# Performance work log

Measured on AMD Instinct MI355X. Metric: run time of the kernel, lower is better.

The kernel has to match this reference:

```python
import jax, jax.numpy as jnp
import numpy as np

B, NORB, N_UP, N_DN, HIDDEN = 1024, 128, 32, 32, 4096


def setup_inputs() -> dict:
    rng = np.random.default_rng(0)
    # Build valid occupancy configs: exactly N_UP up-electrons (bit 0) and
    # N_DN down-electrons (bit 1) per sample. Encoding: 0=empty,1=up,2=dn,3=updn.
    up_order = np.argsort(rng.random((B, NORB)), axis=1)
    dn_order = np.argsort(rng.random((B, NORB)), axis=1)
    up_bit = np.zeros((B, NORB), np.int32)
    dn_bit = np.zeros((B, NORB), np.int32)
    np.put_along_axis(up_bit, up_order[:, :N_UP], 1, axis=1)
    np.put_along_axis(dn_bit, dn_order[:, :N_DN], 1, axis=1)
    x = jnp.asarray(up_bit + 2 * dn_bit, dtype=jnp.int32)

    key = jax.random.key(0)
    k1, k2, k3 = jax.random.split(key, 3)
    orbitals = jax.random.normal(k1, (NORB, N_UP), jnp.float32)
    W1 = jax.random.normal(k2, (4 * NORB, HIDDEN), jnp.float32) / np.sqrt(4 * NORB)
    b1 = jnp.zeros((HIDDEN,), jnp.float32)
    W2 = jax.random.normal(k3, (HIDDEN, NORB * N_UP), jnp.float32) / np.sqrt(HIDDEN)
    b2 = jnp.zeros((NORB * N_UP,), jnp.float32)
    return {"x": x, "orbitals": orbitals, "W1": W1, "b1": b1, "W2": W2, "b2": b2}


def _occupancies_to_electrons(x, n_up, n_dn):
    # Per-spin sorted positions of occupied orbitals. Stable argsort on the
    # inverted mask keeps occupied sites first, in ascending orbital order.
    up_mask = (x & 1) == 1
    dn_mask = (x & 2) == 2
    y_up = jnp.argsort(jnp.where(up_mask, 0, 1), axis=-1, stable=True)[:, :n_up]
    y_dn = jnp.argsort(jnp.where(dn_mask, 0, 1), axis=-1, stable=True)[:, :n_dn]
    return y_up, y_dn


def reference(x, orbitals, W1, b1, W2, b2):
    Bsz, norb = x.shape
    n_up = orbitals.shape[1]

    # correction_fun: MLP on one-hot config -> [B, norb, n_up]
    h = jax.nn.one_hot(x, 4, dtype=W1.dtype).reshape(Bsz, -1)  # [B, 4*norb]
    h = jax.nn.relu(h @ W1 + b1)                               # [B, hidden]
    corrections = (h @ W2 + b2).reshape(Bsz, norb, n_up)       # [B, norb, n_up]

    y_up, y_dn = _occupancies_to_electrons(x, n_up, n_up)
    y_up = y_up[..., None]  # [B, n_up, 1]
    y_dn = y_dn[..., None]

    # gather orbital rows + correction rows per electron (spin-symmetric orbitals)
    phi_up = jnp.take_along_axis(orbitals[None], y_up, axis=1)  # [B, n_up, n_up]
    phi_dn = jnp.take_along_axis(orbitals[None], y_dn, axis=1)
    d_up = jnp.take_along_axis(corrections, y_up, axis=1)
    d_dn = jnp.take_along_axis(corrections, y_dn, axis=1)

    s_up, log_det_up = jnp.linalg.slogdet(phi_up + d_up)
    s_dn, log_det_dn = jnp.linalg.slogdet(phi_dn + d_dn)
    return log_det_up + log_det_dn + jnp.log(s_up * s_dn + 0j)  # complex [B]
```

## Files before the change

kernel.cpp:

```cpp
#include <hip/hip_runtime.h>
#include <cmath>

#define B_SZ  1024
#define NORB  128
#define NUP   32
#define HID   4096
#define NCORR (NORB * NUP)
#define K1    (4 * NORB)

typedef short    bf16x8 __attribute__((ext_vector_type(8)));
typedef _Float16 f16x8  __attribute__((ext_vector_type(8)));
typedef float    f32x4  __attribute__((ext_vector_type(4)));

__device__ __forceinline__ unsigned short f2bf_rne(float f) {
    unsigned int u = __float_as_uint(f);
    u += 0x7FFFu + ((u >> 16) & 1u);
    return (unsigned short)(u >> 16);
}

__global__ __launch_bounds__(256) void k_splitW(const float* __restrict__ W,
                                                unsigned short* __restrict__ Bph,
                                                unsigned short* __restrict__ Bpl,
                                                int ktTot) {
    __shared__ float tile[64][33];
    int n0 = blockIdx.x * 32, k0 = blockIdx.y * 64;
    int t = threadIdx.x;

    int rl = t >> 3, c4 = (t & 7) * 4;
#pragma unroll
    for (int i = 0; i < 2; ++i) {
        int kl = rl + 32 * i;
        float4 v = *(const float4*)(W + (size_t)(k0 + kl) * 4096 + n0 + c4);
        tile[kl][c4 + 0] = v.x; tile[kl][c4 + 1] = v.y;
        tile[kl][c4 + 2] = v.z; tile[kl][c4 + 3] = v.w;
    }
    __syncthreads();

    int nl = t & 31, kg = t >> 5;
    int nt = (n0 + nl) >> 4;
    int kt = (k0 >> 5) + (kg >> 2);
    int lane_o = (kg & 3) * 16 + (nl & 15);
    size_t o = (((size_t)nt * ktTot + kt) * 64 + lane_o) * 8;

    unsigned short hi8[8], lo8[8];
#pragma unroll
    for (int j = 0; j < 8; ++j) {
        float v = tile[kg * 8 + j][nl];
        unsigned short hi = f2bf_rne(v);
        float fhi = __uint_as_float((unsigned int)hi << 16);
        hi8[j] = hi;
        lo8[j] = f2bf_rne(v - fhi);
    }
    *(bf16x8*)(Bph + o) = *(bf16x8*)hi8;
    *(bf16x8*)(Bpl + o) = *(bf16x8*)lo8;
}

__global__ __launch_bounds__(256) void k_splitW16(const float* __restrict__ W,
                                                  _Float16* __restrict__ Bph,
                                                  _Float16* __restrict__ Bpl) {
    __shared__ float tile[64][33];
    int n0 = blockIdx.x * 32, k0 = blockIdx.y * 64;
    int t = threadIdx.x;

    int rl = t >> 3, c4 = (t & 7) * 4;
#pragma unroll
    for (int i = 0; i < 2; ++i) {
        int kl = rl + 32 * i;
        float4 v = *(const float4*)(W + (size_t)(k0 + kl) * 4096 + n0 + c4);
        tile[kl][c4 + 0] = v.x; tile[kl][c4 + 1] = v.y;
        tile[kl][c4 + 2] = v.z; tile[kl][c4 + 3] = v.w;
    }
    __syncthreads();

    int nl = t & 31, kg = t >> 5;
    int nt = (n0 + nl) >> 4;
    int kt = (k0 >> 5) + (kg >> 2);
    int lane_o = (kg & 3) * 16 + (nl & 15);
    size_t o = (((size_t)nt * 128 + kt) * 64 + lane_o) * 8;

    f16x8 hi8, lo8;
#pragma unroll
    for (int j = 0; j < 8; ++j) {
        float v = tile[kg * 8 + j][nl];
        _Float16 hi = (_Float16)v;
        hi8[j] = hi;
        lo8[j] = (_Float16)((v - (float)hi) * 2048.0f);
    }
    *(f16x8*)(Bph + o) = hi8;
    *(f16x8*)(Bpl + o) = lo8;
}

__global__ __launch_bounds__(256, 2) void k_hidden3(const int* __restrict__ x,
                                                    const unsigned short* __restrict__ Bph,
                                                    const unsigned short* __restrict__ Bpl,
                                                    const float* __restrict__ b1,
                                                    _Float16* __restrict__ h16) {
    __shared__ unsigned int sxp[64][8];
    __shared__ unsigned short BF[2][4][4][512];
    __shared__ float Ht[64][132];

    int n0 = blockIdx.x * 128;
    int m0 = blockIdx.y * 64;
    int t = threadIdx.x;
    int w = t >> 6, lane = t & 63;
    int lm = lane & 15, kq = lane >> 4;
    int wn = w * 32;

#pragma unroll
    for (int i = 0; i < 2; ++i) {
        int id = t + 256 * i;
        int row = id >> 3, d = id & 7;
        const int* src = x + (size_t)(m0 + row) * NORB + d * 16;
        unsigned int dw = 0;
#pragma unroll
        for (int b = 0; b < 16; ++b) dw |= ((unsigned int)(src[b] & 3)) << (2 * b);
        sxp[row][d] = dw;
    }

    int nt0 = (n0 + wn) >> 4;
    const unsigned short* bh0 = Bph + (size_t)nt0 * (16 * 512) + (size_t)lane * 8;
    const unsigned short* bh1 = Bph + (size_t)(nt0 + 1) * (16 * 512) + (size_t)lane * 8;
    const unsigned short* bl0 = Bpl + (size_t)nt0 * (16 * 512) + (size_t)lane * 8;
    const unsigned short* bl1 = Bpl + (size_t)(nt0 + 1) * (16 * 512) + (size_t)lane * 8;

    f32x4 acc[4][2] = {};

    bf16x8 r0 = *(const bf16x8*)(bh0);
    bf16x8 r1 = *(const bf16x8*)(bh1);
    bf16x8 r2 = *(const bf16x8*)(bl0);
    bf16x8 r3 = *(const bf16x8*)(bl1);
    bf16x8 r4 = *(const bf16x8*)(bh0 + 512);
    bf16x8 r5 = *(const bf16x8*)(bh1 + 512);
    bf16x8 r6 = *(const bf16x8*)(bl0 + 512);
    bf16x8 r7 = *(const bf16x8*)(bl1 + 512);

    __syncthreads();

    for (int p = 0; p < 8; ++p) {
        if (p) __syncthreads();

        *(bf16x8*)&BF[0][w][0][lane * 8] = r0;
        *(bf16x8*)&BF[0][w][1][lane * 8] = r1;
        *(bf16x8*)&BF[0][w][2][lane * 8] = r2;
        *(bf16x8*)&BF[0][w][3][lane * 8] = r3;
        *(bf16x8*)&BF[1][w][0][lane * 8] = r4;
        *(bf16x8*)&BF[1][w][1][lane * 8] = r5;
        *(bf16x8*)&BF[1][w][2][lane * 8] = r6;
        *(bf16x8*)&BF[1][w][3][lane * 8] = r7;
        __syncthreads();

        int kn = (p + 1 < 8) ? p + 1 : 7;
        r0 = *(const bf16x8*)(bh0 + (2 * kn) * 512);
        r1 = *(const bf16x8*)(bh1 + (2 * kn) * 512);
        r2 = *(const bf16x8*)(bl0 + (2 * kn) * 512);
        r3 = *(const bf16x8*)(bl1 + (2 * kn) * 512);
        r4 = *(const bf16x8*)(bh0 + (2 * kn + 1) * 512);
        r5 = *(const bf16x8*)(bh1 + (2 * kn + 1) * 512);
        r6 = *(const bf16x8*)(bl0 + (2 * kn + 1) * 512);
        r7 = *(const bf16x8*)(bl1 + (2 * kn + 1) * 512);

#pragma unroll
        for (int s = 0; s < 2; ++s) {
            int kt = 2 * p + s;
            int i0 = kt * 8 + kq * 2;
            int dwIdx = i0 >> 4;
            int sh = (i0 & 15) * 2;
            bf16x8 af[4];
#pragma unroll
            for (int fm = 0; fm < 4; ++fm) {
                unsigned int dw = sxp[fm * 16 + lm][dwIdx];
                unsigned int c01 = (dw >> sh) & 0xFu;
                union { bf16x8 v; unsigned long long u[2]; } a;
                a.u[0] = 0x3F80ULL << ((c01 & 3u) * 16);
                a.u[1] = 0x3F80ULL << ((c01 >> 2) * 16);
                af[fm] = a.v;
            }

            bf16x8 b0h = *(const bf16x8*)&BF[s][w][0][lane * 8];
            bf16x8 b1h = *(const bf16x8*)&BF[s][w][1][lane * 8];
            bf16x8 b0l = *(const bf16x8*)&BF[s][w][2][lane * 8];
            bf16x8 b1l = *(const bf16x8*)&BF[s][w][3][lane * 8];

#pragma unroll
            for (int fm = 0; fm < 4; ++fm) {
                acc[fm][0] = __builtin_amdgcn_mfma_f32_16x16x32_bf16(af[fm], b0h, acc[fm][0], 0, 0, 0);
                acc[fm][0] = __builtin_amdgcn_mfma_f32_16x16x32_bf16(af[fm], b0l, acc[fm][0], 0, 0, 0);
                acc[fm][1] = __builtin_amdgcn_mfma_f32_16x16x32_bf16(af[fm], b1h, acc[fm][1], 0, 0, 0);
                acc[fm][1] = __builtin_amdgcn_mfma_f32_16x16x32_bf16(af[fm], b1l, acc[fm][1], 0, 0, 0);
            }
        }
    }

    __syncthreads();
#pragma unroll
    for (int fm = 0; fm < 4; ++fm)
#pragma unroll
        for (int fn = 0; fn < 2; ++fn) {
            int n = wn + fn * 16 + lm;
            float bv = b1[n0 + n];
#pragma unroll
            for (int r = 0; r < 4; ++r)
                Ht[fm * 16 + kq * 4 + r][n] = fmaxf(acc[fm][fn][r] + bv, 0.f);
        }
    __syncthreads();

    size_t mt0 = (size_t)(m0 >> 4), kt0 = (size_t)(n0 >> 5);
#pragma unroll
    for (int fi = 0; fi < 4; ++fi) {
        int f = w * 4 + fi;
        int mt = f >> 2, ktn = f & 3;
        int m = mt * 16 + lm;
        int kn = ktn * 32 + kq * 8;
        float4 v0 = *(const float4*)&Ht[m][kn];
        float4 v1 = *(const float4*)&Ht[m][kn + 4];
        float vv[8] = {v0.x, v0.y, v0.z, v0.w, v1.x, v1.y, v1.z, v1.w};
        f16x8 o16;
#pragma unroll
        for (int j = 0; j < 8; ++j) o16[j] = (_Float16)vv[j];
        size_t o = (((mt0 + mt) * 128 + (kt0 + ktn)) * 64 + lane) * 8;
        *(f16x8*)(h16 + o) = o16;
    }
}

__global__ __launch_bounds__(256) void k_hidden_f32(const int* __restrict__ x,
                                                    const float* __restrict__ W1,
                                                    const float* __restrict__ b1,
                                                    float* __restrict__ h) {
    int b = blockIdx.x, tid = threadIdx.x;
    __shared__ int sx[NORB];
    if (tid < NORB) sx[tid] = x[b * NORB + tid];
    __syncthreads();
    float acc[16];
#pragma unroll
    for (int u = 0; u < 16; ++u) acc[u] = b1[tid + 256 * u];
    for (int i = 0; i < NORB; ++i) {
        const float* row = W1 + (size_t)(4 * i + sx[i]) * HID;
#pragma unroll
        for (int u = 0; u < 16; ++u) acc[u] += row[tid + 256 * u];
    }
    float* hb = h + (size_t)b * HID;
#pragma unroll
    for (int u = 0; u < 16; ++u) hb[tid + 256 * u] = fmaxf(acc[u], 0.f);
}

__global__ __launch_bounds__(256, 2) void k_gemm7(const _Float16* __restrict__ Ap,
                                                  const _Float16* __restrict__ Bph,
                                                  const _Float16* __restrict__ Bpl,
                                                  const float* __restrict__ bias,
                                                  float* __restrict__ C) {
    __shared__ _Float16 AF[2][4][512];

    int n0 = blockIdx.x * 128;
    int m0 = blockIdx.y * 64;
    int t = threadIdx.x;
    int w = t >> 6, lane = t & 63;
    int lm = lane & 15, kq = lane >> 4;
    int wn = w * 32;

    int mt0 = m0 >> 4;
    int nt0 = (n0 + wn) >> 4;

    const _Float16* ag  = Ap  + (size_t)(mt0 + w) * 65536 + (size_t)lane * 8;
    const _Float16* bh0 = Bph + (size_t)nt0 * 65536 + (size_t)lane * 8;
    const _Float16* bh1 = Bph + (size_t)(nt0 + 1) * 65536 + (size_t)lane * 8;
    const _Float16* bl0 = Bpl + (size_t)nt0 * 65536 + (size_t)lane * 8;
    const _Float16* bl1 = Bpl + (size_t)(nt0 + 1) * 65536 + (size_t)lane * 8;

    f32x4 accH[4][2] = {}, accL[4][2] = {};

    f16x8 r0 = *(const f16x8*)(ag);
    f16x8 r1 = *(const f16x8*)(ag + 512);

    for (int ktp = 0; ktp < 64; ++ktp) {
        if (ktp) __syncthreads();

        int o0 = (2 * ktp) * 512, o1 = o0 + 512;
        f16x8 B0h0 = *(const f16x8*)(bh0 + o0);
        f16x8 B0h1 = *(const f16x8*)(bh1 + o0);
        f16x8 B0l0 = *(const f16x8*)(bl0 + o0);
        f16x8 B0l1 = *(const f16x8*)(bl1 + o0);
        f16x8 B1h0 = *(const f16x8*)(bh0 + o1);
        f16x8 B1h1 = *(const f16x8*)(bh1 + o1);
        f16x8 B1l0 = *(const f16x8*)(bl0 + o1);
        f16x8 B1l1 = *(const f16x8*)(bl1 + o1);

        *(f16x8*)&AF[0][w][lane * 8] = r0;
        *(f16x8*)&AF[1][w][lane * 8] = r1;
        __syncthreads();

        int kn = (ktp + 1 < 64) ? ktp + 1 : 63;
        r0 = *(const f16x8*)(ag + (size_t)(2 * kn) * 512);
        r1 = *(const f16x8*)(ag + (size_t)(2 * kn + 1) * 512);

        f16x8 a0[4], a1[4];
#pragma unroll
        for (int fm = 0; fm < 4; ++fm) {
            a0[fm] = *(const f16x8*)&AF[0][fm][lane * 8];
            a1[fm] = *(const f16x8*)&AF[1][fm][lane * 8];
        }

#pragma unroll
        for (int fm = 0; fm < 4; ++fm) {
            accH[fm][0] = __builtin_amdgcn_mfma_f32_16x16x32_f16(a0[fm], B0h0, accH[fm][0], 0, 0, 0);
            accL[fm][0] = __builtin_amdgcn_mfma_f32_16x16x32_f16(a0[fm], B0l0, accL[fm][0], 0, 0, 0);
            accH[fm][1] = __builtin_amdgcn_mfma_f32_16x16x32_f16(a0[fm], B0h1, accH[fm][1], 0, 0, 0);
            accL[fm][1] = __builtin_amdgcn_mfma_f32_16x16x32_f16(a0[fm], B0l1, accL[fm][1], 0, 0, 0);
        }
#pragma unroll
        for (int fm = 0; fm < 4; ++fm) {
            accH[fm][0] = __builtin_amdgcn_mfma_f32_16x16x32_f16(a1[fm], B1h0, accH[fm][0], 0, 0, 0);
            accL[fm][0] = __builtin_amdgcn_mfma_f32_16x16x32_f16(a1[fm], B1l0, accL[fm][0], 0, 0, 0);
            accH[fm][1] = __builtin_amdgcn_mfma_f32_16x16x32_f16(a1[fm], B1h1, accH[fm][1], 0, 0, 0);
            accL[fm][1] = __builtin_amdgcn_mfma_f32_16x16x32_f16(a1[fm], B1l1, accL[fm][1], 0, 0, 0);
        }
    }

    const float ls = 1.0f / 2048.0f;
#pragma unroll
    for (int fm = 0; fm < 4; ++fm)
#pragma unroll
        for (int fn = 0; fn < 2; ++fn) {
            int n = n0 + wn + fn * 16 + lm;
            float bv = bias[n];
#pragma unroll
            for (int r = 0; r < 4; ++r) {
                int m = m0 + fm * 16 + kq * 4 + r;
                C[(size_t)m * NCORR + n] = accH[fm][fn][r] + ls * accL[fm][fn][r] + bv;
            }
        }
}

#define BM 64
#define BN 64
#define BK 32
__global__ __launch_bounds__(256) void k_gemm(const float* __restrict__ A,
                                              const float* __restrict__ Bm,
                                              const float* __restrict__ bias,
                                              float* __restrict__ C) {
    __shared__ float As[BK][68];
    __shared__ float Bs[BK][BN];
    int n0 = blockIdx.x * BN, m0 = blockIdx.y * BM;
    int tid = threadIdx.x;
    int tm = tid >> 4, tn = tid & 15;
    int am = tid >> 3, ak = (tid & 7) * 4;
    int bk = tid >> 4, bn = (tid & 15) * 4;
    float acc[4][4] = {};
    for (int k0 = 0; k0 < HID; k0 += BK) {
#pragma unroll
        for (int s = 0; s < 2; ++s) {
            int m = am + 32 * s;
            float4 v = *(const float4*)(A + (size_t)(m0 + m) * HID + k0 + ak);
            As[ak + 0][m] = v.x; As[ak + 1][m] = v.y;
            As[ak + 2][m] = v.z; As[ak + 3][m] = v.w;
        }
#pragma unroll
        for (int s = 0; s < 2; ++s) {
            int k = bk + 16 * s;
            float4 v = *(const float4*)(Bm + (size_t)(k0 + k) * NCORR + n0 + bn);
            *(float4*)&Bs[k][bn] = v;
        }
        __syncthreads();
#pragma unroll
        for (int kk = 0; kk < BK; ++kk) {
            float4 a = *(const float4*)&As[kk][tm * 4];
            float4 bv = *(const float4*)&Bs[kk][tn * 4];
            float av[4] = {a.x, a.y, a.z, a.w};
            float bb[4] = {bv.x, bv.y, bv.z, bv.w};
#pragma unroll
            for (int i = 0; i < 4; ++i)
#pragma unroll
                for (int j = 0; j < 4; ++j) acc[i][j] += av[i] * bb[j];
        }
        __syncthreads();
    }
#pragma unroll
    for (int i = 0; i < 4; ++i) {
        int m = m0 + tm * 4 + i;
        float4 o;
        o.x = acc[i][0] + bias[n0 + tn * 4 + 0];
        o.y = acc[i][1] + bias[n0 + tn * 4 + 1];
        o.z = acc[i][2] + bias[n0 + tn * 4 + 2];
        o.w = acc[i][3] + bias[n0 + tn * 4 + 3];
        *(float4*)(C + (size_t)m * NCORR + n0 + tn * 4) = o;
    }
}

__global__ __launch_bounds__(128) void k_det(const int* __restrict__ x,
                                             const float* __restrict__ orbitals,
                                             const float* __restrict__ corr,
                                             float* __restrict__ out,
                                             int imag_off) {
    int b = blockIdx.x, tid = threadIdx.x;
    __shared__ int sx[NORB];
    __shared__ int yup[NUP], ydn[NUP];
    __shared__ float M[2][NUP][NUP + 1];
    __shared__ float rlog[2];
    __shared__ int rneg[2];

    sx[tid] = x[b * NORB + tid];
    __syncthreads();

    int occ = sx[tid];
    if (occ & 1) {
        int r = 0;
        for (int i = 0; i < tid; ++i) r += sx[i] & 1;
        yup[r] = tid;
    }
    if (occ & 2) {
        int r = 0;
        for (int i = 0; i < tid; ++i) r += (sx[i] >> 1) & 1;
        ydn[r] = tid;
    }
    __syncthreads();

    const float* cb = corr + (size_t)b * NCORR;
    for (int idx = tid; idx < 2 * NUP * NUP; idx += 128) {
        int s = idx >> 10;
        int i = (idx >> 5) & 31;
        int j = idx & 31;
        int r = s ? ydn[i] : yup[i];
        M[s][i][j] = orbitals[r * NUP + j] + cb[r * NUP + j];
    }
    __syncthreads();

    int wv = tid >> 6, lane = tid & 63;
    float (*Mm)[NUP + 1] = M[wv];
    float logdet = 0.f;
    int neg = 0;

    for (int k = 0; k < NUP; ++k) {
        float v = (lane >= k && lane < NUP) ? fabsf(Mm[lane][k]) : -1.f;
        int pi = lane;
#pragma unroll
        for (int off = 32; off > 0; off >>= 1) {
            float v2 = __shfl_down(v, off);
            int p2 = __shfl_down(pi, off);
            if (v2 > v) { v = v2; pi = p2; }
        }
        int p = __shfl(pi, 0);

        if (p != k) {
            if (lane < NUP) {
                float t1 = Mm[k][lane];
                Mm[k][lane] = Mm[p][lane];
                Mm[p][lane] = t1;
            }
            neg ^= 1;
        }
        __syncthreads();

        float pv = Mm[k][k];
        logdet += logf(fabsf(pv));
        if (pv < 0.f) neg ^= 1;

        int row = k + 1 + (lane & 31);
        int half = lane >> 5;
        if (row < NUP) {
            float f = Mm[row][k] / pv;
            for (int j = k + 1 + half; j < NUP; j += 2)
                Mm[row][j] -= f * Mm[k][j];
        }
        __syncthreads();
    }

    if (lane == 0) { rlog[wv] = logdet; rneg[wv] = neg; }
    __syncthreads();
    if (tid == 0) {
        out[b] = rlog[0] + rlog[1];
        if (imag_off > 0)
            out[imag_off + b] =
                (rneg[0] ^ rneg[1]) ? 3.14159265358979323846f : 0.f;
    }
}

extern "C" void kernel_launch(void* const* d_in, const int* in_sizes, int n_in,
                              void* d_out, int out_size, void* d_ws, size_t ws_size,
                              hipStream_t stream) {
    const int*   x        = (const int*)d_in[0];
    const float* orbitals = (const float*)d_in[1];
    const float* W1       = (const float*)d_in[2];
    const float* b1       = (const float*)d_in[3];
    const float* W2       = (const float*)d_in[4];
    const float* b2       = (const float*)d_in[5];
    float* out = (float*)d_out;
    int imag_off = (out_size == 2 * B_SZ) ? B_SZ : 0;

    const size_t need = (size_t)96 * 1024 * 1024;
    if (ws_size >= need) {
        _Float16* h16  = (_Float16*)d_ws;
        _Float16* Bh16 = h16 + (size_t)B_SZ * HID;
        _Float16* Bl16 = Bh16 + (size_t)HID * NCORR;
        float*    corr = (float*)(Bl16 + (size_t)HID * NCORR);

        unsigned short* W1ph = (unsigned short*)corr;
        unsigned short* W1pl = W1ph + (size_t)K1 * HID;

        k_splitW<<<dim3(HID / 32, K1 / 64), 256, 0, stream>>>(W1, W1ph, W1pl, 16);
        k_splitW16<<<dim3(NCORR / 32, HID / 64), 256, 0, stream>>>(W2, Bh16, Bl16);

        k_hidden3<<<dim3(HID / 128, B_SZ / 64), 256, 0, stream>>>(x, W1ph, W1pl, b1, h16);

        dim3 g2(NCORR / 128, B_SZ / 64);
        k_gemm7<<<g2, 256, 0, stream>>>(h16, Bh16, Bl16, b2, corr);
        k_det<<<B_SZ, 128, 0, stream>>>(x, orbitals, corr, out, imag_off);
    } else {
        float* h    = (float*)d_ws;
        float* corr = h + (size_t)B_SZ * HID;
        k_hidden_f32<<<B_SZ, 256, 0, stream>>>(x, W1, b1, h);
        dim3 g2(NCORR / BN, B_SZ / BM);
        k_gemm<<<g2, 256, 0, stream>>>(h, W2, b2, corr);
        k_det<<<B_SZ, 128, 0, stream>>>(x, orbitals, corr, out, imag_off);
    }
}
```

Measured before the change: 242.5 us.

## Split GEMM block across 8 waves with double-buffered LDS A tiles

The second-layer GEMM now runs 512 threads per block, each wave owning one 16-column N tile instead of two. This halves per-wave accumulators and B-register loads to raise occupancy. The A tile in LDS is double-buffered so one __syncthreads per iteration is enough, and sched_barrier calls pin loads ahead of the MFMA chains, including in the hidden-layer kernel. The cost is more waves sharing each LDS A tile and a less flexible compiler schedule.

```diff
diff --git a/kernel.cpp b/kernel.cpp
--- a/kernel.cpp
+++ b/kernel.cpp
@@ -158,6 +158,7 @@
         r5 = *(const bf16x8*)(bh1 + (2 * kn + 1) * 512);
         r6 = *(const bf16x8*)(bl0 + (2 * kn + 1) * 512);
         r7 = *(const bf16x8*)(bl1 + (2 * kn + 1) * 512);
+        __builtin_amdgcn_sched_barrier(0);
 
 #pragma unroll
         for (int s = 0; s < 2; ++s) {
@@ -243,90 +244,75 @@
     for (int u = 0; u < 16; ++u) hb[tid + 256 * u] = fmaxf(acc[u], 0.f);
 }
 
-__global__ __launch_bounds__(256, 2) void k_gemm7(const _Float16* __restrict__ Ap,
+__global__ __launch_bounds__(512, 4) void k_gemm8(const _Float16* __restrict__ Ap,
                                                   const _Float16* __restrict__ Bph,
                                                   const _Float16* __restrict__ Bpl,
                                                   const float* __restrict__ bias,
                                                   float* __restrict__ C) {
-    __shared__ _Float16 AF[2][4][512];
+    __shared__ _Float16 AF[2][2][4][512];
 
     int n0 = blockIdx.x * 128;
     int m0 = blockIdx.y * 64;
     int t = threadIdx.x;
     int w = t >> 6, lane = t & 63;
     int lm = lane & 15, kq = lane >> 4;
-    int wn = w * 32;
 
     int mt0 = m0 >> 4;
-    int nt0 = (n0 + wn) >> 4;
-
-    const _Float16* ag  = Ap  + (size_t)(mt0 + w) * 65536 + (size_t)lane * 8;
-    const _Float16* bh0 = Bph + (size_t)nt0 * 65536 + (size_t)lane * 8;
-    const _Float16* bh1 = Bph + (size_t)(nt0 + 1) * 65536 + (size_t)lane * 8;
-    const _Float16* bl0 = Bpl + (size_t)nt0 * 65536 + (size_t)lane * 8;
-    const _Float16* bl1 = Bpl + (size_t)(nt0 + 1) * 65536 + (size_t)lane * 8;
-
-    f32x4 accH[4][2] = {}, accL[4][2] = {};
-
-    f16x8 r0 = *(const f16x8*)(ag);
-    f16x8 r1 = *(const f16x8*)(ag + 512);
+    int nt0 = (n0 >> 4) + w;
+
+    int sA = w & 1, mA = w >> 1;
+    const _Float16* ag = Ap  + (size_t)(mt0 + mA) * 65536 + (size_t)lane * 8;
+    const _Float16* bh = Bph + (size_t)nt0 * 65536 + (size_t)lane * 8;
+    const _Float16* bl = Bpl + (size_t)nt0 * 65536 + (size_t)lane * 8;
+
+    f32x4 accH[4] = {}, accL[4] = {};
+
+    f16x8 r = *(const f16x8*)(ag + (size_t)sA * 512);
 
     for (int ktp = 0; ktp < 64; ++ktp) {
-        if (ktp) __syncthreads();
-
-        int o0 = (2 * ktp) * 512, o1 = o0 + 512;
-        f16x8 B0h0 = *(const f16x8*)(bh0 + o0);
-        f16x8 B0h1 = *(const f16x8*)(bh1 + o0);
-        f16x8 B0l0 = *(const f16x8*)(bl0 + o0);
-        f16x8 B0l1 = *(const f16x8*)(bl1 + o0);
-        f16x8 B1h0 = *(const f16x8*)(bh0 + o1);
-        f16x8 B1h1 = *(const f16x8*)(bh1 + o1);
-        f16x8 B1l0 = *(const f16x8*)(bl0 + o1);
-        f16x8 B1l1 = *(const f16x8*)(bl1 + o1);
-
-        *(f16x8*)&AF[0][w][lane * 8] = r0;
-        *(f16x8*)&AF[1][w][lane * 8] = r1;
+        int buf = ktp & 1;
+        *(f16x8*)&AF[buf][sA][mA][lane * 8] = r;
         __syncthreads();
 
+        size_t oc = (size_t)(2 * ktp) * 512;
+        f16x8 B0h = *(const f16x8*)(bh + oc);
+        f16x8 B0l = *(const f16x8*)(bl + oc);
+        f16x8 B1h = *(const f16x8*)(bh + oc + 512);
+        f16x8 B1l = *(const f16x8*)(bl + oc + 512);
         int kn = (ktp + 1 < 64) ? ktp + 1 : 63;
-        r0 = *(const f16x8*)(ag + (size_t)(2 * kn) * 512);
-        r1 = *(const f16x8*)(ag + (size_t)(2 * kn + 1) * 512);
+        f16x8 nr = *(const f16x8*)(ag + (size_t)(2 * kn + sA) * 512);
+        __builtin_amdgcn_sched_barrier(0);
 
         f16x8 a0[4], a1[4];
 #pragma unroll
         for (int fm = 0; fm < 4; ++fm) {
-            a0[fm] = *(const f16x8*)&AF[0][fm][lane * 8];
-            a1[fm] = *(const f16x8*)&AF[1][fm][lane * 8];
+            a0[fm] = *(const f16x8*)&AF[buf][0][fm][lane * 8];
+            a1[fm] = *(const f16x8*)&AF[buf][1][fm][lane * 8];
         }
 
 #pragma unroll
         for (int fm = 0; fm < 4; ++fm) {
-            accH[fm][0] = __builtin_amdgcn_mfma_f32_16x16x32_f16(a0[fm], B0h0, accH[fm][0], 0, 0, 0);
-            accL[fm][0] = __builtin_amdgcn_mfma_f32_16x16x32_f16(a0[fm], B0l0, accL[fm][0], 0, 0, 0);
-            accH[fm][1] = __builtin_amdgcn_mfma_f32_16x16x32_f16(a0[fm], B0h1, accH[fm][1], 0, 0, 0);
-            accL[fm][1] = __builtin_amdgcn_mfma_f32_16x16x32_f16(a0[fm], B0l1, accL[fm][1], 0, 0, 0);
+            accH[fm] = __builtin_amdgcn_mfma_f32_16x16x32_f16(a0[fm], B0h, accH[fm], 0, 0, 0);
+            accL[fm] = __builtin_amdgcn_mfma_f32_16x16x32_f16(a0[fm], B0l, accL[fm], 0, 0, 0);
         }
 #pragma unroll
         for (int fm = 0; fm < 4; ++fm) {
-            accH[fm][0] = __builtin_amdgcn_mfma_f32_16x16x32_f16(a1[fm], B1h0, accH[fm][0], 0, 0, 0);
-            accL[fm][0] = __builtin_amdgcn_mfma_f32_16x16x32_f16(a1[fm], B1l0, accL[fm][0], 0, 0, 0);
-            accH[fm][1] = __builtin_amdgcn_mfma_f32_16x16x32_f16(a1[fm], B1h1, accH[fm][1], 0, 0, 0);
-            accL[fm][1] = __builtin_amdgcn_mfma_f32_16x16x32_f16(a1[fm], B1l1, accL[fm][1], 0, 0, 0);
-        }
+            accH[fm] = __builtin_amdgcn_mfma_f32_16x16x32_f16(a1[fm], B1h, accH[fm], 0, 0, 0);
+            accL[fm] = __builtin_amdgcn_mfma_f32_16x16x32_f16(a1[fm], B1l, accL[fm], 0, 0, 0);
+        }
+
+        r = nr;
     }
 
     const float ls = 1.0f / 2048.0f;
+    int n = n0 + w * 16 + lm;
+    float bv = bias[n];
 #pragma unroll
     for (int fm = 0; fm < 4; ++fm)
 #pragma unroll
-        for (int fn = 0; fn < 2; ++fn) {
-            int n = n0 + wn + fn * 16 + lm;
-            float bv = bias[n];
-#pragma unroll
-            for (int r = 0; r < 4; ++r) {
-                int m = m0 + fm * 16 + kq * 4 + r;
-                C[(size_t)m * NCORR + n] = accH[fm][fn][r] + ls * accL[fm][fn][r] + bv;
-            }
+        for (int rr = 0; rr < 4; ++rr) {
+            int m = m0 + fm * 16 + kq * 4 + rr;
+            C[(size_t)m * NCORR + n] = accH[fm][rr] + ls * accL[fm][rr] + bv;
         }
 }
 
@@ -501,7 +487,7 @@
         k_hidden3<<<dim3(HID / 128, B_SZ / 64), 256, 0, stream>>>(x, W1ph, W1pl, b1, h16);
 
         dim3 g2(NCORR / 128, B_SZ / 64);
-        k_gemm7<<<g2, 256, 0, stream>>>(h16, Bh16, Bl16, b2, corr);
+        k_gemm8<<<g2, 512, 0, stream>>>(h16, Bh16, Bl16, b2, corr);
         k_det<<<B_SZ, 128, 0, stream>>>(x, orbitals, corr, out, imag_off);
     } else {
         float* h    = (float*)d_ws;
```

Measured after the change: 241.2 us. About the same (-0.5%).
